# Optimization experiments

Hardware: AMD Instinct MI355X
Metric: run time of the kernel (lower is better)

The kernel has to match this reference:

```python
import jax, jax.numpy as jnp
import numpy as np

D_MODEL = 512
D_ATTN = 128


def setup_inputs() -> dict:
    key = jax.random.key(0)
    k1, k2, k3, k4, k5 = jax.random.split(key, 5)
    B, N = 4, 4096
    x = jax.random.normal(k1, (B, N, D_MODEL), dtype=jnp.float32)
    key_mask = jnp.ones((B, N, 1), dtype=jnp.float32)
    # nn.Linear params (stored as [in, out] for x @ W)
    W_qkv = jax.random.normal(k2, (D_MODEL, 3 * D_ATTN), dtype=jnp.float32) / np.sqrt(D_MODEL)
    b_qkv = jax.random.normal(k3, (3 * D_ATTN,), dtype=jnp.float32) * 0.01
    W_out = jax.random.normal(k4, (D_ATTN, D_MODEL), dtype=jnp.float32) / np.sqrt(D_ATTN)
    b_out = jax.random.normal(k5, (D_MODEL,), dtype=jnp.float32) * 0.01
    return {"x": x, "key_mask": key_mask, "W_qkv": W_qkv, "b_qkv": b_qkv,
            "W_out": W_out, "b_out": b_out}


def reference(x, key_mask, W_qkv, b_qkv, W_out, b_out):
    # Fused QKV projection: [B, N, 3*d_attn]
    qkv = jnp.einsum('bnd,de->bne', x, W_qkv) + b_qkv
    q, k, v = jnp.split(qkv, 3, axis=-1)  # each [B, N, d_attn]
    d_attn = q.shape[-1]
    scale = 1.0 / np.sqrt(d_attn)
    # Full [B, N, N] score matrix (faithful to original einsum)
    scores = jnp.einsum('bnd,bmd->bnm', q, k)
    # Causal mask applied BEFORE scaling (as in original: mask, then *scale)
    N = x.shape[1]
    causal = jnp.tril(jnp.ones((N, N), dtype=bool))  # True = keep
    scores = jnp.where(causal[None, :, :], scores, -jnp.inf)
    scores = scores * scale
    attn = jax.nn.softmax(scores, axis=-1)  # dropout is identity in eval
    out = jnp.einsum('bnm,bmd->bnd', attn, v)
    out = out * key_mask  # broadcast [B, N, 1]
    out = jnp.einsum('bnd,de->bne', out, W_out) + b_out
    return out
```

## Files before the change

kernel.cpp:

```cpp
#include <hip/hip_runtime.h>
#include <hip/hip_bf16.h>
#include <math.h>

typedef __attribute__((ext_vector_type(4))) float f32x4;
typedef __attribute__((ext_vector_type(4))) float fvec4;
typedef __attribute__((ext_vector_type(8))) short bf16x8_t;
typedef __attribute__((ext_vector_type(4))) short bf16x4_t;

static constexpr int BATCH = 4;
static constexpr int SEQ = 4096;
static constexpr int DM = 512;
static constexpr int DA = 128;
static constexpr int BN = BATCH * SEQ;
static constexpr int IPB = 187;
static constexpr int N_ITEMS = BATCH * IPB;

static constexpr float MASKV = -3.0e38f;
static constexpr float MINIT = -1.0e30f;

static __device__ __forceinline__ unsigned short f2bf(float f) {
  unsigned u = __builtin_bit_cast(unsigned, f);
  u += 0x7fffu + ((u >> 16) & 1u);
  return (unsigned short)(u >> 16);
}
static __device__ __forceinline__ float bf2f(unsigned short u) {
  return __builtin_bit_cast(float, ((unsigned)u) << 16);
}
static __device__ __forceinline__ float fexp2(float x) {
#if __has_builtin(__builtin_amdgcn_exp2f)
  return __builtin_amdgcn_exp2f(x);
#else
  return exp2f(x);
#endif
}
static __device__ __forceinline__ unsigned pkbf(float lo, float hi) {
  unsigned r;
  asm("v_cvt_pk_bf16_f32 %0, %1, %2" : "=v"(r) : "v"(lo), "v"(hi));
  return r;
}

#define GLDS16(gsrc, ldst)                                                        \
  __builtin_amdgcn_global_load_lds(                                               \
      (const __attribute__((address_space(1))) void*)(gsrc),                      \
      (__attribute__((address_space(3))) void*)(ldst), 16, 0, 0)

static constexpr float QSC = 0.08838834764831845f * 1.4426950408889634f;

__global__ __launch_bounds__(256) void prep_w_kernel(
    const float* __restrict__ Wqkv, const float* __restrict__ Wout,
    unsigned short* __restrict__ WqT, unsigned short* __restrict__ WoT) {
  int t = blockIdx.x * 256 + threadIdx.x;
  if (t < 512 * 384) {
    int k = t / 384, n = t - k * 384;
    WqT[n * 512 + k] = f2bf(Wqkv[t]);
  }
  if (t < 128 * 512) {
    int k = t >> 9, n = t & 511;
    WoT[n * 128 + k] = f2bf(Wout[t]);
  }
}

__global__ __launch_bounds__(512, 4) void qkv_kernel(
    const float* __restrict__ x, const unsigned short* __restrict__ WqT,
    const float* __restrict__ bias, unsigned short* __restrict__ qbf,
    unsigned short* __restrict__ kpk, unsigned short* __restrict__ vpk) {
  __shared__ unsigned short Alds[128 * 64];
  __shared__ unsigned short Blds[128 * 64];

  const int m0 = blockIdx.x * 128;
  const int n0 = blockIdx.y * 128;
  const int tid = threadIdx.x;
  const int wave = tid >> 6, lane = tid & 63;
  const int g = lane >> 4, lr = lane & 15;
  const int wm = wave >> 2, wn = wave & 3;

  const int srow = lane >> 3;
  const int sslot = lane & 7;
  const int sksw = ((sslot ^ srow) * 8);

  f32x4 acc[4][2] = {};

  for (int kb = 0; kb < DM; kb += 64) {
    __syncthreads();
#pragma unroll
    for (int i = 0; i < 2; ++i) {
      int ch = wave * 2 + i;
      GLDS16(&WqT[(size_t)(n0 + ch * 8 + srow) * DM + kb + sksw],
             (char*)Blds + ch * 1024);
    }
    fvec4 af32[2][2];
#pragma unroll
    for (int i = 0; i < 2; ++i) {
      int ch = wave * 2 + i;
      const float* ap = &x[(size_t)(m0 + ch * 8 + srow) * DM + kb + sksw];
      af32[i][0] = *(const fvec4*)ap;
      af32[i][1] = *(const fvec4*)(ap + 4);
    }
#pragma unroll
    for (int i = 0; i < 2; ++i) {
      int ch = wave * 2 + i;
      union { unsigned u[4]; bf16x8_t v; } pk;
      pk.u[0] = pkbf(af32[i][0][0], af32[i][0][1]);
      pk.u[1] = pkbf(af32[i][0][2], af32[i][0][3]);
      pk.u[2] = pkbf(af32[i][1][0], af32[i][1][1]);
      pk.u[3] = pkbf(af32[i][1][2], af32[i][1][3]);
      *(bf16x8_t*)&Alds[ch * 512 + lane * 8] = pk.v;
    }
    asm volatile("s_waitcnt vmcnt(0)" ::: "memory");
    __syncthreads();

#pragma unroll
    for (int c2 = 0; c2 < 2; ++c2) {
      bf16x8_t ar[4], br[2];
#pragma unroll
      for (int mi = 0; mi < 4; ++mi) {
        int row = wm * 64 + mi * 16 + lr;
        ar[mi] = *(const bf16x8_t*)&Alds[row * 64 + (((c2 * 4 + g) ^ (row & 7)) * 8)];
      }
#pragma unroll
      for (int ni = 0; ni < 2; ++ni) {
        int row = wn * 32 + ni * 16 + lr;
        br[ni] = *(const bf16x8_t*)&Blds[row * 64 + (((c2 * 4 + g) ^ (row & 7)) * 8)];
      }
#pragma unroll
      for (int mi = 0; mi < 4; ++mi)
#pragma unroll
        for (int ni = 0; ni < 2; ++ni)
          acc[mi][ni] = __builtin_amdgcn_mfma_f32_16x16x32_bf16(ar[mi], br[ni],
                                                                acc[mi][ni], 0, 0, 0);
    }
  }

  if (n0 == 0) {
#pragma unroll
    for (int ni = 0; ni < 2; ++ni) {
      int col = wn * 32 + ni * 16 + lr;
      float bv = bias[col];
#pragma unroll
      for (int mi = 0; mi < 4; ++mi) {
        int tokb = m0 + wm * 64 + mi * 16 + 4 * g;
#pragma unroll
        for (int r = 0; r < 4; ++r)
          qbf[(size_t)(tokb + r) * DA + col] = f2bf((acc[mi][ni][r] + bv) * QSC);
      }
    }
  } else if (n0 == 128) {
#pragma unroll
    for (int ni = 0; ni < 2; ++ni) {
      int kd = wn * 32 + ni * 16 + lr;
      float bv = bias[128 + kd];
      int unit = (kd >> 5) * 4 + ((kd >> 3) & 3);
      int elem = kd & 7;
#pragma unroll
      for (int mi = 0; mi < 4; ++mi) {
        int tokb = m0 + wm * 64 + mi * 16 + 4 * g;
#pragma unroll
        for (int r = 0; r < 4; ++r) {
          int token = tokb + r;
          int tile32 = token >> 5;
          int u = (((token >> 4) & 1) * 16) + unit;
          kpk[(size_t)tile32 * 4096 + u * 128 + (token & 15) * 8 + elem] =
              f2bf(acc[mi][ni][r] + bv);
        }
      }
    }
  } else {
#pragma unroll
    for (int mi = 0; mi < 4; ++mi) {
      int keyb = m0 + wm * 64 + mi * 16 + 4 * g;
      int tile32 = keyb >> 5;
      int kl0 = keyb & 31;
      int gp = (kl0 >> 2) & 3;
      int jhi = kl0 >> 4;
#pragma unroll
      for (int ni = 0; ni < 2; ++ni) {
        int d = wn * 32 + ni * 16 + lr;
        float bv = bias[256 + d];
        union { bf16x4_t v; unsigned short u[4]; } pk;
#pragma unroll
        for (int r = 0; r < 4; ++r) pk.u[r] = f2bf(acc[mi][ni][r] + bv);
        int unit = (d >> 4) * 4 + gp;
        *(bf16x4_t*)&vpk[(size_t)tile32 * 4096 + unit * 128 + (d & 15) * 8 + jhi * 4] =
            pk.v;
      }
    }
  }
}

static __device__ __forceinline__ void softmax64(
    f32x4 s[4], float& m_r, float& l_r, f32x4* oacc, bf16x8_t pb[2]) {
  float tmax = MASKV;
#pragma unroll
  for (int ct = 0; ct < 4; ++ct)
#pragma unroll
    for (int r = 0; r < 4; ++r) tmax = fmaxf(tmax, s[ct][r]);
  tmax = fmaxf(tmax, __shfl_xor(tmax, 16, 64));
  tmax = fmaxf(tmax, __shfl_xor(tmax, 32, 64));
  if (!__all(tmax <= m_r + 10.0f)) {
    float mn = fmaxf(m_r, tmax);
    float al = fexp2(m_r - mn);
    m_r = mn;
    l_r *= al;
#pragma unroll
    for (int t = 0; t < 8; ++t)
#pragma unroll
      for (int r = 0; r < 4; ++r) oacc[t][r] *= al;
  }
  float rs = 0.f;
#pragma unroll
  for (int ct = 0; ct < 4; ++ct)
#pragma unroll
    for (int r = 0; r < 4; ++r) {
      float p = fexp2(s[ct][r] - m_r);
      s[ct][r] = p;
      rs += p;
    }
  rs += __shfl_xor(rs, 16, 64);
  rs += __shfl_xor(rs, 32, 64);
  l_r += rs;
#pragma unroll
  for (int h = 0; h < 2; ++h) {
    union { unsigned u[4]; bf16x8_t v; } pk;
    pk.u[0] = pkbf(s[2 * h][0], s[2 * h][1]);
    pk.u[1] = pkbf(s[2 * h][2], s[2 * h][3]);
    pk.u[2] = pkbf(s[2 * h + 1][0], s[2 * h + 1][1]);
    pk.u[3] = pkbf(s[2 * h + 1][2], s[2 * h + 1][3]);
    pb[h] = pk.v;
  }
}

__global__ __launch_bounds__(256, 3) void attn_kernel(
    const unsigned short* __restrict__ qbf, const unsigned short* __restrict__ kpk,
    const unsigned short* __restrict__ vpk, const float* __restrict__ key_mask,
    unsigned short* __restrict__ part_o, float* __restrict__ part_ml,
    unsigned short* __restrict__ ctx) {
  __shared__ unsigned short Klds[2][8192];
  __shared__ unsigned short Vlds[8192];

  const int flat = blockIdx.x;
  const int b = flat & 3;
  const int idxr = flat >> 2;
  int rem = idxr;
  int qb = 31;
  for (;;) {
    int nc = (qb + 3) / 3;
    if (rem < nc) break;
    rem -= nc;
    --qb;
  }
  const int ci = rem;
  const bool direct = (qb < 3);
  const int key0 = ci * 384;
  const int nkeys = min(384, (qb + 1) * 128 - key0);
  const int nt = nkeys >> 6;

  const int tid = threadIdx.x;
  const int wave = tid >> 6, lane = tid & 63;
  const int g = lane >> 4, lr = lane & 15;
  const int q0 = wave * 16 + lr;
  const int q1 = q0 + 64;

  bf16x8_t qf0[4], qf1[4];
  {
    const unsigned short* qbase = qbf + ((size_t)(b * SEQ + qb * 128)) * DA + g * 8;
#pragma unroll
    for (int c = 0; c < 4; ++c) {
      qf0[c] = *(const bf16x8_t*)(qbase + (size_t)q0 * DA + c * 32);
      qf1[c] = *(const bf16x8_t*)(qbase + (size_t)q1 * DA + c * 32);
    }
  }

  f32x4 oacc0[8] = {}, oacc1[8] = {};
  float m0r = MINIT, l0 = 0.f, m1r = MINIT, l1 = 0.f;

  const int t32b = b * 128 + ci * 12;
  const unsigned short* ksrc = kpk + (size_t)t32b * 4096 + wave * 2048 + lane * 8;
  const unsigned short* vsrc = vpk + (size_t)t32b * 4096 + wave * 2048 + lane * 8;

#define STAGEK(buf, tt)                                                      \
  do {                                                                       \
    char* kd_ = (char*)Klds[buf] + wave * 4096;                              \
    _Pragma("unroll")                                                        \
    for (int i_ = 0; i_ < 4; ++i_)                                           \
      GLDS16(ksrc + (size_t)(tt) * 8192 + i_ * 512, kd_ + i_ * 1024);        \
  } while (0)
#define STAGEV(tt)                                                           \
  do {                                                                       \
    char* vd_ = (char*)Vlds + wave * 4096;                                   \
    _Pragma("unroll")                                                        \
    for (int i_ = 0; i_ < 4; ++i_)                                           \
      GLDS16(vsrc + (size_t)(tt) * 8192 + i_ * 512, vd_ + i_ * 1024);        \
  } while (0)

  STAGEK(0, 0);

  for (int tt = 0; tt < nt; ++tt) {
    const int cur = tt & 1;
    STAGEV(tt);
    if (tt + 1 < nt) {
      STAGEK(cur ^ 1, tt + 1);
      asm volatile("s_waitcnt vmcnt(8)" ::: "memory");
    } else {
      asm volatile("s_waitcnt vmcnt(4)" ::: "memory");
    }
    __builtin_amdgcn_s_barrier();
    __builtin_amdgcn_sched_barrier(0);

    f32x4 s0[4] = {}, s1[4] = {};
    __builtin_amdgcn_s_setprio(1);
#pragma unroll
    for (int ct = 0; ct < 4; ++ct)
#pragma unroll
      for (int c = 0; c < 4; ++c) {
        bf16x8_t kf = *(const bf16x8_t*)&Klds[cur][(ct >> 1) * 4096 +
                                                   (((ct & 1) * 16 + c * 4 + g) * 16 + lr) * 8];
        s0[ct] = __builtin_amdgcn_mfma_f32_16x16x32_bf16(kf, qf0[c], s0[ct], 0, 0, 0);
        s1[ct] = __builtin_amdgcn_mfma_f32_16x16x32_bf16(kf, qf1[c], s1[ct], 0, 0, 0);
      }
    __builtin_amdgcn_s_setprio(0);

    const int koff = key0 + tt * 64 - qb * 128;
    if (koff + 63 > wave * 16) {
      int thr = q0 - koff;
#pragma unroll
      for (int ct = 0; ct < 4; ++ct)
#pragma unroll
        for (int r = 0; r < 4; ++r)
          if (16 * ct + 4 * g + r > thr) s0[ct][r] = MASKV;
    }
    if (koff + 63 > 64 + wave * 16) {
      int thr = q1 - koff;
#pragma unroll
      for (int ct = 0; ct < 4; ++ct)
#pragma unroll
        for (int r = 0; r < 4; ++r)
          if (16 * ct + 4 * g + r > thr) s1[ct][r] = MASKV;
    }

    bf16x8_t pb0[2], pb1[2];
    softmax64(s0, m0r, l0, oacc0, pb0);
    softmax64(s1, m1r, l1, oacc1, pb1);

    if (tt + 1 < nt) {
      asm volatile("s_waitcnt vmcnt(4)" ::: "memory");
    } else {
      asm volatile("s_waitcnt vmcnt(0)" ::: "memory");
    }
    __builtin_amdgcn_s_barrier();
    __builtin_amdgcn_sched_barrier(0);

    __builtin_amdgcn_s_setprio(1);
#pragma unroll
    for (int t = 0; t < 8; ++t)
#pragma unroll
      for (int h = 0; h < 2; ++h) {
        bf16x8_t vf = *(const bf16x8_t*)&Vlds[h * 4096 + ((t * 4 + g) * 16 + lr) * 8];
        oacc0[t] = __builtin_amdgcn_mfma_f32_16x16x32_bf16(vf, pb0[h], oacc0[t], 0, 0, 0);
        oacc1[t] = __builtin_amdgcn_mfma_f32_16x16x32_bf16(vf, pb1[h], oacc1[t], 0, 0, 0);
      }
    __builtin_amdgcn_s_setprio(0);

    __builtin_amdgcn_s_barrier();
  }
#undef STAGEK
#undef STAGEV

  const int slot = b * IPB + idxr;
#pragma unroll
  for (int grp = 0; grp < 2; ++grp) {
    const int row = grp ? q1 : q0;
    const f32x4* oa = grp ? oacc1 : oacc0;
    const float mr = grp ? m1r : m0r;
    const float lr_ = grp ? l1 : l0;
    if (direct) {
      float km = key_mask[b * SEQ + qb * 128 + row];
      float inv = km / lr_;
      unsigned short* co = ctx + ((size_t)(b * SEQ + qb * 128 + row)) * DA;
#pragma unroll
      for (int t = 0; t < 8; ++t) {
        union { bf16x4_t v; unsigned short u[4]; } pk;
#pragma unroll
        for (int r = 0; r < 4; ++r) pk.u[r] = f2bf(oa[t][r] * inv);
        *(bf16x4_t*)&co[t * 16 + 4 * g] = pk.v;
      }
    } else {
      unsigned short* po = part_o + (size_t)slot * 16384 + (size_t)row * 128;
#pragma unroll
      for (int t = 0; t < 8; ++t) {
        union { bf16x4_t v; unsigned short u[4]; } pk;
#pragma unroll
        for (int r = 0; r < 4; ++r) pk.u[r] = f2bf(oa[t][r]);
        *(bf16x4_t*)&po[t * 16 + 4 * g] = pk.v;
      }
      if (g == 0) {
        float2 ml = make_float2(mr, lr_);
        *(float2*)&part_ml[((size_t)slot * 128 + row) * 2] = ml;
      }
    }
  }
}

__global__ __launch_bounds__(512) void combine_kernel(
    const unsigned short* __restrict__ part_o, const float* __restrict__ part_ml,
    const float* __restrict__ key_mask, unsigned short* __restrict__ ctx) {
  const int qb = 3 + (blockIdx.x >> 2);
  const int rq = blockIdx.x & 3;
  const int b = blockIdx.y;
  const int nc = (qb + 3) / 3;
  int idx0 = 0;
  for (int q = 31; q > qb; --q) idx0 += (q + 3) / 3;
  const int row = rq * 32 + (threadIdx.x >> 4);
  const int cs = threadIdx.x & 15;

  float m = MINIT;
  for (int ci = 0; ci < nc; ++ci) {
    int slot = b * IPB + idx0 + ci;
    m = fmaxf(m, part_ml[((size_t)slot * 128 + row) * 2 + 0]);
  }
  float l = 0.f;
  float acc[8];
#pragma unroll
  for (int k = 0; k < 8; ++k) acc[k] = 0.f;
  for (int ci = 0; ci < nc; ++ci) {
    int slot = b * IPB + idx0 + ci;
    float mi = part_ml[((size_t)slot * 128 + row) * 2 + 0];
    float li = part_ml[((size_t)slot * 128 + row) * 2 + 1];
    float w = fexp2(mi - m);
    l += w * li;
    const unsigned short* po =
        part_o + (size_t)slot * 16384 + (size_t)row * 128 + cs * 8;
    bf16x8_t v = *(const bf16x8_t*)po;
#pragma unroll
    for (int jj = 0; jj < 8; ++jj) acc[jj] += w * bf2f((unsigned short)v[jj]);
  }
  int rowg = b * SEQ + qb * 128 + row;
  float sc = key_mask[rowg] / l;
  union { bf16x8_t v; unsigned short u[8]; } pk;
#pragma unroll
  for (int jj = 0; jj < 8; ++jj) pk.u[jj] = f2bf(acc[jj] * sc);
  *(bf16x8_t*)&ctx[(size_t)rowg * 128 + cs * 8] = pk.v;
}

__global__ __launch_bounds__(512, 4) void outproj_kernel(
    const unsigned short* __restrict__ ctx, const unsigned short* __restrict__ WoT,
    const float* __restrict__ bias, float* __restrict__ out) {
  __shared__ unsigned short Alds[128 * 64];
  __shared__ unsigned short Blds[128 * 64];

  const int m0 = blockIdx.x * 128;
  const int n0 = blockIdx.y * 128;
  const int tid = threadIdx.x;
  const int wave = tid >> 6, lane = tid & 63;
  const int g = lane >> 4, lr = lane & 15;
  const int wm = wave >> 2, wn = wave & 3;

  const int srow = lane >> 3;
  const int sslot = lane & 7;
  const int sksw = ((sslot ^ srow) * 8);

  f32x4 acc[4][2] = {};

  for (int kb = 0; kb < DA; kb += 64) {
    __syncthreads();
#pragma unroll
    for (int i = 0; i < 2; ++i) {
      int ch = wave * 2 + i;
      GLDS16(&ctx[(size_t)(m0 + ch * 8 + srow) * DA + kb + sksw],
             (char*)Alds + ch * 1024);
      GLDS16(&WoT[(size_t)(n0 + ch * 8 + srow) * DA + kb + sksw],
             (char*)Blds + ch * 1024);
    }
    asm volatile("s_waitcnt vmcnt(0)" ::: "memory");
    __syncthreads();

#pragma unroll
    for (int c2 = 0; c2 < 2; ++c2) {
      bf16x8_t ar[4], br[2];
#pragma unroll
      for (int mi = 0; mi < 4; ++mi) {
        int row = wm * 64 + mi * 16 + lr;
        ar[mi] = *(const bf16x8_t*)&Alds[row * 64 + (((c2 * 4 + g) ^ (row & 7)) * 8)];
      }
#pragma unroll
      for (int ni = 0; ni < 2; ++ni) {
        int row = wn * 32 + ni * 16 + lr;
        br[ni] = *(const bf16x8_t*)&Blds[row * 64 + (((c2 * 4 + g) ^ (row & 7)) * 8)];
      }
#pragma unroll
      for (int mi = 0; mi < 4; ++mi)
#pragma unroll
        for (int ni = 0; ni < 2; ++ni)
          acc[mi][ni] = __builtin_amdgcn_mfma_f32_16x16x32_bf16(ar[mi], br[ni],
                                                                acc[mi][ni], 0, 0, 0);
    }
  }

#pragma unroll
  for (int ni = 0; ni < 2; ++ni) {
    int col = n0 + wn * 32 + ni * 16 + lr;
    float bv = bias[col];
#pragma unroll
    for (int mi = 0; mi < 4; ++mi) {
      int tokb = m0 + wm * 64 + mi * 16 + 4 * g;
#pragma unroll
      for (int r = 0; r < 4; ++r)
        out[(size_t)(tokb + r) * DM + col] = acc[mi][ni][r] + bv;
    }
  }
}

extern "C" void kernel_launch(void* const* d_in, const int* in_sizes, int n_in,
                              void* d_out, int out_size, void* d_ws, size_t ws_size,
                              hipStream_t stream) {
  const float* x = (const float*)d_in[0];
  const float* key_mask = (const float*)d_in[1];
  const float* W_qkv = (const float*)d_in[2];
  const float* b_qkv = (const float*)d_in[3];
  const float* W_out = (const float*)d_in[4];
  const float* b_out = (const float*)d_in[5];
  float* out = (float*)d_out;

  unsigned short* ws = (unsigned short*)d_ws;
  unsigned short* qbf = ws;
  unsigned short* kpk = qbf + (size_t)BN * DA;
  unsigned short* vpk = kpk + (size_t)BN * DA;
  unsigned short* ctx = vpk + (size_t)BN * DA;
  unsigned short* xbf = ctx + (size_t)BN * DA;
  unsigned short* WqT = xbf + (size_t)BN * DM;
  unsigned short* WoT = WqT + (size_t)384 * 512;
  unsigned short* part_o = WoT + (size_t)512 * 128;
  float* part_ml = (float*)(part_o + (size_t)N_ITEMS * 16384);

  prep_w_kernel<<<dim3(768), 256, 0, stream>>>(W_qkv, W_out, WqT, WoT);
  qkv_kernel<<<dim3(BN / 128, 3), 512, 0, stream>>>(x, WqT, b_qkv, qbf, kpk, vpk);
  attn_kernel<<<dim3(N_ITEMS), 256, 0, stream>>>(qbf, kpk, vpk, key_mask,
                                                 part_o, part_ml, ctx);
  combine_kernel<<<dim3(29 * 4, 4), 512, 0, stream>>>(part_o, part_ml, key_mask, ctx);
  outproj_kernel<<<dim3(BN / 128, 4), 512, 0, stream>>>(ctx, WoT, b_out, out);
}
```

Measured before the change: 72.85 us.

## Double-buffer LDS tiles in QKV projection GEMM to overlap loads with MFMA

Converts the QKV projection kernel's A and B shared-memory tiles to double buffers. The next K-slice's global loads (x into registers, weights via direct-to-LDS) are issued before the current slice's MFMA work, so load latency is hidden and one barrier per iteration is removed. Doubling LDS to 64KB per block may cut occupancy given launch_bounds(512,4). The QKV kernel is only one stage of the whole attention pipeline.

```diff
diff --git a/kernel.cpp b/kernel.cpp
--- a/kernel.cpp
+++ b/kernel.cpp
@@ -64,8 +64,8 @@
     const float* __restrict__ x, const unsigned short* __restrict__ WqT,
     const float* __restrict__ bias, unsigned short* __restrict__ qbf,
     unsigned short* __restrict__ kpk, unsigned short* __restrict__ vpk) {
-  __shared__ unsigned short Alds[128 * 64];
-  __shared__ unsigned short Blds[128 * 64];
+  __shared__ unsigned short Alds[2][128 * 64];
+  __shared__ unsigned short Blds[2][128 * 64];
 
   const int m0 = blockIdx.x * 128;
   const int n0 = blockIdx.y * 128;
@@ -79,35 +79,54 @@
   const int sksw = ((sslot ^ srow) * 8);
 
   f32x4 acc[4][2] = {};
-
-  for (int kb = 0; kb < DM; kb += 64) {
-    __syncthreads();
-#pragma unroll
-    for (int i = 0; i < 2; ++i) {
-      int ch = wave * 2 + i;
-      GLDS16(&WqT[(size_t)(n0 + ch * 8 + srow) * DM + kb + sksw],
-             (char*)Blds + ch * 1024);
-    }
-    fvec4 af32[2][2];
-#pragma unroll
-    for (int i = 0; i < 2; ++i) {
-      int ch = wave * 2 + i;
-      const float* ap = &x[(size_t)(m0 + ch * 8 + srow) * DM + kb + sksw];
-      af32[i][0] = *(const fvec4*)ap;
-      af32[i][1] = *(const fvec4*)(ap + 4);
-    }
-#pragma unroll
-    for (int i = 0; i < 2; ++i) {
-      int ch = wave * 2 + i;
-      union { unsigned u[4]; bf16x8_t v; } pk;
-      pk.u[0] = pkbf(af32[i][0][0], af32[i][0][1]);
-      pk.u[1] = pkbf(af32[i][0][2], af32[i][0][3]);
-      pk.u[2] = pkbf(af32[i][1][0], af32[i][1][1]);
-      pk.u[3] = pkbf(af32[i][1][2], af32[i][1][3]);
-      *(bf16x8_t*)&Alds[ch * 512 + lane * 8] = pk.v;
-    }
-    asm volatile("s_waitcnt vmcnt(0)" ::: "memory");
-    __syncthreads();
+  fvec4 af32[2][2];
+
+#define LOADA(kb_)                                                             \
+  do {                                                                         \
+    _Pragma("unroll")                                                          \
+    for (int i_ = 0; i_ < 2; ++i_) {                                           \
+      int ch_ = wave * 2 + i_;                                                 \
+      const float* ap_ = &x[(size_t)(m0 + ch_ * 8 + srow) * DM + (kb_) + sksw];\
+      af32[i_][0] = *(const fvec4*)ap_;                                        \
+      af32[i_][1] = *(const fvec4*)(ap_ + 4);                                  \
+    }                                                                          \
+  } while (0)
+#define STAGEB(buf_, kb_)                                                      \
+  do {                                                                         \
+    _Pragma("unroll")                                                          \
+    for (int i_ = 0; i_ < 2; ++i_) {                                           \
+      int ch_ = wave * 2 + i_;                                                 \
+      GLDS16(&WqT[(size_t)(n0 + ch_ * 8 + srow) * DM + (kb_) + sksw],          \
+             (char*)Blds[buf_] + ch_ * 1024);                                  \
+    }                                                                          \
+  } while (0)
+#define WRITEA(buf_)                                                           \
+  do {                                                                         \
+    _Pragma("unroll")                                                          \
+    for (int i_ = 0; i_ < 2; ++i_) {                                           \
+      int ch_ = wave * 2 + i_;                                                 \
+      union { unsigned u[4]; bf16x8_t v; } pk_;                                \
+      pk_.u[0] = pkbf(af32[i_][0][0], af32[i_][0][1]);                         \
+      pk_.u[1] = pkbf(af32[i_][0][2], af32[i_][0][3]);                         \
+      pk_.u[2] = pkbf(af32[i_][1][0], af32[i_][1][1]);                         \
+      pk_.u[3] = pkbf(af32[i_][1][2], af32[i_][1][3]);                         \
+      *(bf16x8_t*)&Alds[buf_][ch_ * 512 + lane * 8] = pk_.v;                   \
+    }                                                                          \
+  } while (0)
+
+  LOADA(0);
+  STAGEB(0, 0);
+  WRITEA(0);
+  asm volatile("s_waitcnt vmcnt(0) lgkmcnt(0)" ::: "memory");
+  __builtin_amdgcn_s_barrier();
+  __builtin_amdgcn_sched_barrier(0);
+
+  for (int k = 0; k < 8; ++k) {
+    const int cur = k & 1;
+    if (k < 7) {
+      LOADA((k + 1) * 64);
+      STAGEB(cur ^ 1, (k + 1) * 64);
+    }
 
 #pragma unroll
     for (int c2 = 0; c2 < 2; ++c2) {
@@ -115,12 +134,12 @@
 #pragma unroll
       for (int mi = 0; mi < 4; ++mi) {
         int row = wm * 64 + mi * 16 + lr;
-        ar[mi] = *(const bf16x8_t*)&Alds[row * 64 + (((c2 * 4 + g) ^ (row & 7)) * 8)];
+        ar[mi] = *(const bf16x8_t*)&Alds[cur][row * 64 + (((c2 * 4 + g) ^ (row & 7)) * 8)];
       }
 #pragma unroll
       for (int ni = 0; ni < 2; ++ni) {
         int row = wn * 32 + ni * 16 + lr;
-        br[ni] = *(const bf16x8_t*)&Blds[row * 64 + (((c2 * 4 + g) ^ (row & 7)) * 8)];
+        br[ni] = *(const bf16x8_t*)&Blds[cur][row * 64 + (((c2 * 4 + g) ^ (row & 7)) * 8)];
       }
 #pragma unroll
       for (int mi = 0; mi < 4; ++mi)
@@ -129,7 +148,17 @@
           acc[mi][ni] = __builtin_amdgcn_mfma_f32_16x16x32_bf16(ar[mi], br[ni],
                                                                 acc[mi][ni], 0, 0, 0);
     }
-  }
+
+    if (k < 7) {
+      WRITEA(cur ^ 1);
+      asm volatile("s_waitcnt vmcnt(0) lgkmcnt(0)" ::: "memory");
+      __builtin_amdgcn_s_barrier();
+      __builtin_amdgcn_sched_barrier(0);
+    }
+  }
+#undef LOADA
+#undef STAGEB
+#undef WRITEA
 
   if (n0 == 0) {
 #pragma unroll
```

Result: no change. 72.99 us (+0.2%).
